# Kernel tuning notes

Hardware: AMD Instinct MI355X
Metric: run time of the kernel (lower is better)

Reference implementation:

```python
import jax, jax.numpy as jnp
import numpy as np

NUM_BINS = 50


def _power_spectrum(x):
    # fft2 over last two dims, |.|^2, fftshift — matches torch.fft.fft2/fftshift
    freq = jnp.fft.fft2(x, axes=(-2, -1))
    power = jnp.abs(freq) ** 2
    return jnp.fft.fftshift(power, axes=(-2, -1))


def _radial_bin_ids(H, W, num_bins):
    # Static precompute of the bin index for every pixel (replaces the
    # triple-nested mask loop with a single segment reduction).
    cy, cx = H // 2, W // 2
    y = jnp.arange(H, dtype=jnp.float32) - cy
    x = jnp.arange(W, dtype=jnp.float32) - cx
    radius = jnp.sqrt(y[:, None] ** 2 + x[None, :] ** 2)  # [H, W]
    max_radius = min(H, W) // 2
    bin_edges = jnp.linspace(0.0, float(max_radius), num_bins + 1)
    # bin i covers [edges[i], edges[i+1]); radius >= max_radius -> overflow bin
    ids = jnp.clip(jnp.searchsorted(bin_edges, radius.ravel(), side='right') - 1, 0, num_bins)
    return ids  # [H*W], values in [0, num_bins] (num_bins = dropped overflow)


def _radial_profile(power, num_bins=NUM_BINS):
    B, C, H, W = power.shape
    ids = _radial_bin_ids(H, W, num_bins)
    pflat = power.reshape(B, C, H * W)
    seg_sum = jax.vmap(jax.vmap(lambda p: jax.ops.segment_sum(p, ids, num_segments=num_bins + 1)))(pflat)
    counts = jax.ops.segment_sum(jnp.ones((H * W,), power.dtype), ids, num_segments=num_bins + 1)
    profile = jnp.where(counts > 0, seg_sum / jnp.maximum(counts, 1.0), 0.0)
    return profile[..., :num_bins]  # [B, C, num_bins]


def setup_inputs() -> dict:
    key = jax.random.key(0)
    k1, k2 = jax.random.split(key)
    x = jax.random.normal(k1, (16, 3, 512, 512), dtype=jnp.float32)
    reference = jax.random.normal(k2, (16, 3, 512, 512), dtype=jnp.float32)
    return {"x": x, "reference": reference}


def reference(x, reference):
    power_x = _power_spectrum(x)
    profile_x = _radial_profile(power_x)
    power_ref = _power_spectrum(reference)
    profile_ref = _radial_profile(power_ref)
    B = profile_x.shape[0]
    logits_x = profile_x.reshape(B, -1)
    logits_ref = profile_ref.reshape(B, -1)
    # F.kl_div(log_p, q).sum(1) == sum q * (log q - log p)
    log_p = jax.nn.log_softmax(logits_x, axis=1)
    log_q = jax.nn.log_softmax(logits_ref, axis=1)
    q = jnp.exp(log_q)
    divergence = jnp.sum(q * (log_q - log_p), axis=1)  # [B]
    return divergence
```

## Files before the change

### kernel.cpp

```cpp
#include <hip/hip_runtime.h>


#define NIMG 96
#define NB 50
#define NCOL 257
#define PHYS(k) ((k) ^ (((k) >> 3) & 7))

typedef unsigned int uint32;
typedef unsigned short ushort16;

__device__ __forceinline__ float2 cadd(float2 a, float2 b){ return make_float2(a.x+b.x, a.y+b.y); }
__device__ __forceinline__ float2 csub(float2 a, float2 b){ return make_float2(a.x-b.x, a.y-b.y); }
__device__ __forceinline__ float2 cmul(float2 a, float2 b){
  return make_float2(fmaf(a.x, b.x, -(a.y*b.y)), fmaf(a.x, b.y, a.y*b.x));
}
__device__ __forceinline__ float2 mul_mi(float2 a){ return make_float2(a.y, -a.x); }

__device__ __forceinline__ uint32 bfpack(float re, float im) {
  uint32 ur = __float_as_uint(re); ur += 0x7FFFu + ((ur >> 16) & 1u);
  uint32 ui = __float_as_uint(im); ui += 0x7FFFu + ((ui >> 16) & 1u);
  return (ur & 0xFFFF0000u) | (ui >> 16);
}
__device__ __forceinline__ float2 bfunpack(uint32 u) {
  return make_float2(__uint_as_float(u & 0xFFFF0000u), __uint_as_float(u << 16));
}

struct C8 { float2 m0, m1, m2, m3, m4, m5, m6, m7; };

__device__ __forceinline__ C8 fft8(C8 v) {
  const float C = 0.70710678118654752f;
  float2 t0=cadd(v.m0,v.m4), t1=csub(v.m0,v.m4);
  float2 t2=cadd(v.m2,v.m6), t3m=mul_mi(csub(v.m2,v.m6));
  float2 E0=cadd(t0,t2), E1=cadd(t1,t3m), E2=csub(t0,t2), E3=csub(t1,t3m);
  float2 s0=cadd(v.m1,v.m5), s1=csub(v.m1,v.m5);
  float2 s2=cadd(v.m3,v.m7), s3m=mul_mi(csub(v.m3,v.m7));
  float2 O0=cadd(s0,s2), O1=cadd(s1,s3m), O2=csub(s0,s2), O3=csub(s1,s3m);
  O1 = make_float2(C*(O1.x+O1.y), C*(O1.y-O1.x));
  O2 = mul_mi(O2);
  O3 = make_float2(C*(O3.y-O3.x), -C*(O3.x+O3.y));
  C8 r;
  r.m0=cadd(E0,O0); r.m4=csub(E0,O0);
  r.m1=cadd(E1,O1); r.m5=csub(E1,O1);
  r.m2=cadd(E2,O2); r.m6=csub(E2,O2);
  r.m3=cadd(E3,O3); r.m7=csub(E3,O3);
  return r;
}

#define TWAPPLY(XA, XB, W) do { float2 t_ = (W);                        \
  XA.m1=cmul(XA.m1,t_); XB.m1=cmul(XB.m1,t_); t_=cmul(t_,(W));          \
  XA.m2=cmul(XA.m2,t_); XB.m2=cmul(XB.m2,t_); t_=cmul(t_,(W));          \
  XA.m3=cmul(XA.m3,t_); XB.m3=cmul(XB.m3,t_); t_=cmul(t_,(W));          \
  XA.m4=cmul(XA.m4,t_); XB.m4=cmul(XB.m4,t_); t_=cmul(t_,(W));          \
  XA.m5=cmul(XA.m5,t_); XB.m5=cmul(XB.m5,t_); t_=cmul(t_,(W));          \
  XA.m6=cmul(XA.m6,t_); XB.m6=cmul(XB.m6,t_); t_=cmul(t_,(W));          \
  XA.m7=cmul(XA.m7,t_); XB.m7=cmul(XB.m7,t_); } while(0)

#define TWAP1(X, W) do { float2 t_ = (W);                               \
  X.m1=cmul(X.m1,t_); t_=cmul(t_,(W));                                  \
  X.m2=cmul(X.m2,t_); t_=cmul(t_,(W));                                  \
  X.m3=cmul(X.m3,t_); t_=cmul(t_,(W));                                  \
  X.m4=cmul(X.m4,t_); t_=cmul(t_,(W));                                  \
  X.m5=cmul(X.m5,t_); t_=cmul(t_,(W));                                  \
  X.m6=cmul(X.m6,t_); t_=cmul(t_,(W));                                  \
  X.m7=cmul(X.m7,t_); } while(0)

#define DUAL_FFT512(XA, XB, ZA, ZB, W1, W2, HI, LO) do {                      \
  XA = fft8(XA); XB = fft8(XB);                                               \
  TWAPPLY(XA, XB, W1);                                                        \
  ZA[      8*((HI)^0)+(LO)] = XA.m0;  ZB[      8*((HI)^0)+(LO)] = XB.m0;      \
  ZA[ 64 + 8*((HI)^1)+(LO)] = XA.m1;  ZB[ 64 + 8*((HI)^1)+(LO)] = XB.m1;      \
  ZA[128 + 8*((HI)^2)+(LO)] = XA.m2;  ZB[128 + 8*((HI)^2)+(LO)] = XB.m2;      \
  ZA[192 + 8*((HI)^3)+(LO)] = XA.m3;  ZB[192 + 8*((HI)^3)+(LO)] = XB.m3;      \
  ZA[256 + 8*((HI)^4)+(LO)] = XA.m4;  ZB[256 + 8*((HI)^4)+(LO)] = XB.m4;      \
  ZA[320 + 8*((HI)^5)+(LO)] = XA.m5;  ZB[320 + 8*((HI)^5)+(LO)] = XB.m5;      \
  ZA[384 + 8*((HI)^6)+(LO)] = XA.m6;  ZB[384 + 8*((HI)^6)+(LO)] = XB.m6;      \
  ZA[448 + 8*((HI)^7)+(LO)] = XA.m7;  ZB[448 + 8*((HI)^7)+(LO)] = XB.m7;      \
  __builtin_amdgcn_wave_barrier();                                            \
  XA.m0 = ZA[64*(HI)+8*(0^(HI))+(LO)]; XB.m0 = ZB[64*(HI)+8*(0^(HI))+(LO)];   \
  XA.m1 = ZA[64*(HI)+8*(1^(HI))+(LO)]; XB.m1 = ZB[64*(HI)+8*(1^(HI))+(LO)];   \
  XA.m2 = ZA[64*(HI)+8*(2^(HI))+(LO)]; XB.m2 = ZB[64*(HI)+8*(2^(HI))+(LO)];   \
  XA.m3 = ZA[64*(HI)+8*(3^(HI))+(LO)]; XB.m3 = ZB[64*(HI)+8*(3^(HI))+(LO)];   \
  XA.m4 = ZA[64*(HI)+8*(4^(HI))+(LO)]; XB.m4 = ZB[64*(HI)+8*(4^(HI))+(LO)];   \
  XA.m5 = ZA[64*(HI)+8*(5^(HI))+(LO)]; XB.m5 = ZB[64*(HI)+8*(5^(HI))+(LO)];   \
  XA.m6 = ZA[64*(HI)+8*(6^(HI))+(LO)]; XB.m6 = ZB[64*(HI)+8*(6^(HI))+(LO)];   \
  XA.m7 = ZA[64*(HI)+8*(7^(HI))+(LO)]; XB.m7 = ZB[64*(HI)+8*(7^(HI))+(LO)];   \
  __builtin_amdgcn_wave_barrier();                                            \
  XA = fft8(XA); XB = fft8(XB);                                               \
  TWAPPLY(XA, XB, W2);                                                        \
  ZA[64*(HI)+8*(0^(HI))+((LO)^0)] = XA.m0; ZB[64*(HI)+8*(0^(HI))+((LO)^0)] = XB.m0; \
  ZA[64*(HI)+8*(1^(HI))+((LO)^1)] = XA.m1; ZB[64*(HI)+8*(1^(HI))+((LO)^1)] = XB.m1; \
  ZA[64*(HI)+8*(2^(HI))+((LO)^2)] = XA.m2; ZB[64*(HI)+8*(2^(HI))+((LO)^2)] = XB.m2; \
  ZA[64*(HI)+8*(3^(HI))+((LO)^3)] = XA.m3; ZB[64*(HI)+8*(3^(HI))+((LO)^3)] = XB.m3; \
  ZA[64*(HI)+8*(4^(HI))+((LO)^4)] = XA.m4; ZB[64*(HI)+8*(4^(HI))+((LO)^4)] = XB.m4; \
  ZA[64*(HI)+8*(5^(HI))+((LO)^5)] = XA.m5; ZB[64*(HI)+8*(5^(HI))+((LO)^5)] = XB.m5; \
  ZA[64*(HI)+8*(6^(HI))+((LO)^6)] = XA.m6; ZB[64*(HI)+8*(6^(HI))+((LO)^6)] = XB.m6; \
  ZA[64*(HI)+8*(7^(HI))+((LO)^7)] = XA.m7; ZB[64*(HI)+8*(7^(HI))+((LO)^7)] = XB.m7; \
  __builtin_amdgcn_wave_barrier();                                            \
  XA.m0 = ZA[64*(HI)+8*((LO)^(HI))+(0^(LO))]; XB.m0 = ZB[64*(HI)+8*((LO)^(HI))+(0^(LO))]; \
  XA.m1 = ZA[64*(HI)+8*((LO)^(HI))+(1^(LO))]; XB.m1 = ZB[64*(HI)+8*((LO)^(HI))+(1^(LO))]; \
  XA.m2 = ZA[64*(HI)+8*((LO)^(HI))+(2^(LO))]; XB.m2 = ZB[64*(HI)+8*((LO)^(HI))+(2^(LO))]; \
  XA.m3 = ZA[64*(HI)+8*((LO)^(HI))+(3^(LO))]; XB.m3 = ZB[64*(HI)+8*((LO)^(HI))+(3^(LO))]; \
  XA.m4 = ZA[64*(HI)+8*((LO)^(HI))+(4^(LO))]; XB.m4 = ZB[64*(HI)+8*((LO)^(HI))+(4^(LO))]; \
  XA.m5 = ZA[64*(HI)+8*((LO)^(HI))+(5^(LO))]; XB.m5 = ZB[64*(HI)+8*((LO)^(HI))+(5^(LO))]; \
  XA.m6 = ZA[64*(HI)+8*((LO)^(HI))+(6^(LO))]; XB.m6 = ZB[64*(HI)+8*((LO)^(HI))+(6^(LO))]; \
  XA.m7 = ZA[64*(HI)+8*((LO)^(HI))+(7^(LO))]; XB.m7 = ZB[64*(HI)+8*((LO)^(HI))+(7^(LO))]; \
  __builtin_amdgcn_wave_barrier();                                            \
  XA = fft8(XA); XB = fft8(XB);                                               \
} while(0)

#define FFT512_1(X, Z, W1, W2, HI, LO) do {                                   \
  X = fft8(X);                                                                \
  TWAP1(X, W1);                                                               \
  Z[      8*((HI)^0)+(LO)] = X.m0;                                            \
  Z[ 64 + 8*((HI)^1)+(LO)] = X.m1;                                            \
  Z[128 + 8*((HI)^2)+(LO)] = X.m2;                                            \
  Z[192 + 8*((HI)^3)+(LO)] = X.m3;                                            \
  Z[256 + 8*((HI)^4)+(LO)] = X.m4;                                            \
  Z[320 + 8*((HI)^5)+(LO)] = X.m5;                                            \
  Z[384 + 8*((HI)^6)+(LO)] = X.m6;                                            \
  Z[448 + 8*((HI)^7)+(LO)] = X.m7;                                            \
  __builtin_amdgcn_wave_barrier();                                            \
  X.m0 = Z[64*(HI)+8*(0^(HI))+(LO)];                                          \
  X.m1 = Z[64*(HI)+8*(1^(HI))+(LO)];                                          \
  X.m2 = Z[64*(HI)+8*(2^(HI))+(LO)];                                          \
  X.m3 = Z[64*(HI)+8*(3^(HI))+(LO)];                                          \
  X.m4 = Z[64*(HI)+8*(4^(HI))+(LO)];                                          \
  X.m5 = Z[64*(HI)+8*(5^(HI))+(LO)];                                          \
  X.m6 = Z[64*(HI)+8*(6^(HI))+(LO)];                                          \
  X.m7 = Z[64*(HI)+8*(7^(HI))+(LO)];                                          \
  __builtin_amdgcn_wave_barrier();                                            \
  X = fft8(X);                                                                \
  TWAP1(X, W2);                                                               \
  Z[64*(HI)+8*(0^(HI))+((LO)^0)] = X.m0;                                      \
  Z[64*(HI)+8*(1^(HI))+((LO)^1)] = X.m1;                                      \
  Z[64*(HI)+8*(2^(HI))+((LO)^2)] = X.m2;                                      \
  Z[64*(HI)+8*(3^(HI))+((LO)^3)] = X.m3;                                      \
  Z[64*(HI)+8*(4^(HI))+((LO)^4)] = X.m4;                                      \
  Z[64*(HI)+8*(5^(HI))+((LO)^5)] = X.m5;                                      \
  Z[64*(HI)+8*(6^(HI))+((LO)^6)] = X.m6;                                      \
  Z[64*(HI)+8*(7^(HI))+((LO)^7)] = X.m7;                                      \
  __builtin_amdgcn_wave_barrier();                                            \
  X.m0 = Z[64*(HI)+8*((LO)^(HI))+(0^(LO))];                                   \
  X.m1 = Z[64*(HI)+8*((LO)^(HI))+(1^(LO))];                                   \
  X.m2 = Z[64*(HI)+8*((LO)^(HI))+(2^(LO))];                                   \
  X.m3 = Z[64*(HI)+8*((LO)^(HI))+(3^(LO))];                                   \
  X.m4 = Z[64*(HI)+8*((LO)^(HI))+(4^(LO))];                                   \
  X.m5 = Z[64*(HI)+8*((LO)^(HI))+(5^(LO))];                                   \
  X.m6 = Z[64*(HI)+8*((LO)^(HI))+(6^(LO))];                                   \
  X.m7 = Z[64*(HI)+8*((LO)^(HI))+(7^(LO))];                                   \
  __builtin_amdgcn_wave_barrier();                                            \
  X = fft8(X);                                                                \
} while(0)

#define TWIDDLE_W(W1, W2, lane)                                             \
  float2 W1, W2;                                                            \
  {                                                                         \
    float sv, cv;                                                           \
    __sincosf(-6.283185307179586f * (float)(lane) / 512.f, &sv, &cv);       \
    W1 = make_float2(cv, sv);                                               \
    __sincosf(-6.283185307179586f * (float)((lane) & 7) / 64.f, &sv, &cv);  \
    W2 = make_float2(cv, sv);                                               \
  }

__device__ __forceinline__ int binOf(int s, int cc) {
  return (int)(sqrtf((float)(s * s + cc * cc)) * 0.1953125f);
}
__device__ __forceinline__ int slo(int b, int cc) {
  if (b <= 0) return 0;
  float t = 26.2144f * (float)(b * b) - (float)(cc * cc);
  int s = (t <= 0.f) ? 0 : (int)ceilf(sqrtf(t));
  if (s > 257) s = 257;
  while (s > 0 && binOf(s - 1, cc) >= b) --s;
  while (s < 257 && binOf(s, cc) < b) ++s;
  return s;
}

__global__ __launch_bounds__(256) void build_slo_table(ushort16* __restrict__ tab)
{
  const int idx = blockIdx.x * 256 + threadIdx.x;
  if (idx >= NCOL * 51) return;
  const int c = idx / 51, b = idx - c * 51;
  tab[c * 52 + b] = (ushort16)slo(b, c);
}

__global__ __launch_bounds__(256, 4) void fft_rows_T(
    const float* __restrict__ xin, const float* __restrict__ rin,
    uint32* __restrict__ outT, int img0)
{
  __shared__ float2 s_z[8][512];
  __shared__ uint2  s_stage[64][8];
  const int tid = threadIdx.x, w = tid >> 6, lane = tid & 63;
  const int hi = lane >> 3, lo = lane & 7;
  const int imgL = blockIdx.x >> 5, blkin = blockIdx.x & 31;
  const int img = img0 + imgL;
  const float* base = (img < 48) ? (xin + (size_t)img * 262144)
                                 : (rin + (size_t)(img - 48) * 262144);
  const int rpA = blkin * 8 + w;
  const int rpB = rpA + 4;
  const float* srcA = base + (size_t)rpA * 1024;
  const float* srcB = base + (size_t)rpB * 1024;

  TWIDDLE_W(w1, w2, lane)
  float2* zA = s_z[2*w];
  float2* zB = s_z[2*w + 1];
  uint32* outImg = outT + (size_t)imgL * ((size_t)NCOL * 512);

  C8 xA, xB;
  xA.m0 = make_float2(srcA[      lane], srcA[512 +       lane]);
  xA.m1 = make_float2(srcA[ 64 + lane], srcA[512 +  64 + lane]);
  xA.m2 = make_float2(srcA[128 + lane], srcA[512 + 128 + lane]);
  xA.m3 = make_float2(srcA[192 + lane], srcA[512 + 192 + lane]);
  xA.m4 = make_float2(srcA[256 + lane], srcA[512 + 256 + lane]);
  xA.m5 = make_float2(srcA[320 + lane], srcA[512 + 320 + lane]);
  xA.m6 = make_float2(srcA[384 + lane], srcA[512 + 384 + lane]);
  xA.m7 = make_float2(srcA[448 + lane], srcA[512 + 448 + lane]);
  xB.m0 = make_float2(srcB[      lane], srcB[512 +       lane]);
  xB.m1 = make_float2(srcB[ 64 + lane], srcB[512 +  64 + lane]);
  xB.m2 = make_float2(srcB[128 + lane], srcB[512 + 128 + lane]);
  xB.m3 = make_float2(srcB[192 + lane], srcB[512 + 192 + lane]);
  xB.m4 = make_float2(srcB[256 + lane], srcB[512 + 256 + lane]);
  xB.m5 = make_float2(srcB[320 + lane], srcB[512 + 320 + lane]);
  xB.m6 = make_float2(srcB[384 + lane], srcB[512 + 384 + lane]);
  xB.m7 = make_float2(srcB[448 + lane], srcB[512 + 448 + lane]);

  DUAL_FFT512(xA, xB, zA, zB, w1, w2, hi, lo);

  zA[PHYS(hi + 8*lo +   0)] = xA.m0;  zB[PHYS(hi + 8*lo +   0)] = xB.m0;
  zA[PHYS(hi + 8*lo +  64)] = xA.m1;  zB[PHYS(hi + 8*lo +  64)] = xB.m1;
  zA[PHYS(hi + 8*lo + 128)] = xA.m2;  zB[PHYS(hi + 8*lo + 128)] = xB.m2;
  zA[PHYS(hi + 8*lo + 192)] = xA.m3;  zB[PHYS(hi + 8*lo + 192)] = xB.m3;
  zA[PHYS(hi + 8*lo + 256)] = xA.m4;  zB[PHYS(hi + 8*lo + 256)] = xB.m4;
  zA[PHYS(hi + 8*lo + 320)] = xA.m5;  zB[PHYS(hi + 8*lo + 320)] = xB.m5;
  zA[PHYS(hi + 8*lo + 384)] = xA.m6;  zB[PHYS(hi + 8*lo + 384)] = xB.m6;
  zA[PHYS(hi + 8*lo + 448)] = xA.m7;  zB[PHYS(hi + 8*lo + 448)] = xB.m7;
  __builtin_amdgcn_wave_barrier();

  #pragma unroll
  for (int a = 0; a < 4; ++a) {
    const int k  = 64 * a + lane;
    const int pk = (512 - k) & 511;
    float2 zkA = zA[PHYS(k)], zpA = zA[PHYS(pk)];
    float2 zkB = zB[PHYS(k)], zpB = zB[PHYS(pk)];
    uint32 uA0 = bfpack(0.5f*(zkA.x + zpA.x), 0.5f*(zkA.y - zpA.y));
    uint32 uA1 = bfpack(0.5f*(zkA.y + zpA.y), 0.5f*(zpA.x - zkA.x));
    uint32 uB0 = bfpack(0.5f*(zkB.x + zpB.x), 0.5f*(zkB.y - zpB.y));
    uint32 uB1 = bfpack(0.5f*(zkB.y + zpB.y), 0.5f*(zpB.x - zkB.x));
    s_stage[lane][(w + lane) & 7]     = make_uint2(uA0, uA1);
    s_stage[lane][(w + 4 + lane) & 7] = make_uint2(uB0, uB1);
    __syncthreads();
    const int kk = tid >> 2, jj = (tid & 3) * 2;
    uint2 v0 = s_stage[kk][(jj + kk) & 7];
    uint2 v1 = s_stage[kk][(jj + 1 + kk) & 7];
    *reinterpret_cast<uint4*>(outImg + ((size_t)(64*a + kk) * 512
                                        + 16*blkin + 2*jj)) =
        make_uint4(v0.x, v0.y, v1.x, v1.y);
    __syncthreads();
  }
  if (lane == 0) {
    float2 znA = zA[256], znB = zB[256];
    *reinterpret_cast<uint2*>(outImg + ((size_t)256 * 512 + 2 * rpA)) =
        make_uint2(bfpack(znA.x, 0.f), bfpack(znA.y, 0.f));
    *reinterpret_cast<uint2*>(outImg + ((size_t)256 * 512 + 2 * rpB)) =
        make_uint2(bfpack(znB.x, 0.f), bfpack(znB.y, 0.f));
  }
}

__global__ __launch_bounds__(256, 8) void fft_cols_bin1(
    const uint32* __restrict__ inT, const ushort16* __restrict__ tab,
    float* __restrict__ profSum, int img0)
{
  __shared__ float2 s_z[4][512];
  __shared__ float s_bins[4][64];
  const int tid = threadIdx.x, w = tid >> 6, lane = tid & 63;
  const int hi = lane >> 3, lo = lane & 7;
  const int imgL = blockIdx.x / 65, blkin = blockIdx.x - imgL * 65;
  const int imgG = img0 + imgL;
  const int c  = blkin * 4 + w;
  const int cs = (c <= 256) ? c : 256;
  const float wf = (c > 256) ? 0.f : ((c == 0 || c == 256) ? 1.f : 2.f);

  TWIDDLE_W(w1, w2, lane)
  float2* z = s_z[w];
  const uint32* src = inT + ((size_t)(imgL * NCOL + cs)) * 512;
  C8 x;
  x.m0 = bfunpack(src[      lane]);
  x.m1 = bfunpack(src[ 64 + lane]);
  x.m2 = bfunpack(src[128 + lane]);
  x.m3 = bfunpack(src[192 + lane]);
  x.m4 = bfunpack(src[256 + lane]);
  x.m5 = bfunpack(src[320 + lane]);
  x.m6 = bfunpack(src[384 + lane]);
  x.m7 = bfunpack(src[448 + lane]);

  int ts0 = 0, ts1 = 0;
  if (lane < NB) {
    ts0 = tab[cs * 52 + lane];
    ts1 = tab[cs * 52 + lane + 1];
  }

  FFT512_1(x, z, w1, w2, hi, lo);

  float* zf = (float*)z;
  const int low6 = hi + 8 * lo;
  zf[low6      ] = x.m0.x*x.m0.x + x.m0.y*x.m0.y;
  zf[low6 +  64] = x.m1.x*x.m1.x + x.m1.y*x.m1.y;
  zf[low6 + 128] = x.m2.x*x.m2.x + x.m2.y*x.m2.y;
  zf[low6 + 192] = x.m3.x*x.m3.x + x.m3.y*x.m3.y;
  zf[low6 + 256] = x.m4.x*x.m4.x + x.m4.y*x.m4.y;
  zf[low6 + 320] = x.m5.x*x.m5.x + x.m5.y*x.m5.y;
  zf[low6 + 384] = x.m6.x*x.m6.x + x.m6.y*x.m6.y;
  zf[low6 + 448] = x.m7.x*x.m7.x + x.m7.y*x.m7.y;
  __builtin_amdgcn_wave_barrier();

  float4 a0 = *reinterpret_cast<float4*>(&zf[8 * lane]);
  float4 a1 = *reinterpret_cast<float4*>(&zf[8 * lane + 4]);

  a0.y += a0.x; a0.z += a0.y; a0.w += a0.z;
  a1.x += a0.w; a1.y += a1.x; a1.z += a1.y; a1.w += a1.z;
  float tot = a1.w;

  float s = tot;
  #pragma unroll
  for (int d = 1; d < 64; d <<= 1) {
    float t = __shfl_up(s, d);
    if (lane >= d) s += t;
  }
  float off = s - tot;
  a0.x += off; a0.y += off; a0.z += off; a0.w += off;
  a1.x += off; a1.y += off; a1.z += off; a1.w += off;

  *reinterpret_cast<float4*>(&zf[8 * lane])     = a0;
  *reinterpret_cast<float4*>(&zf[8 * lane + 4]) = a1;
  __builtin_amdgcn_wave_barrier();

  float acc = 0.f;
  if (lane < NB) {
    const int s0 = ts0, s1 = ts1;
    int hp = (s1 < 257 ? s1 : 257) - 1;
    float pos = ((hp >= 0) ? zf[hp] : 0.f) - ((s0 > 0) ? zf[s0 - 1] : 0.f);
    int sa = (s0 > 1) ? s0 : 1;
    int sb = (s1 - 1 < 255) ? (s1 - 1) : 255;
    float neg = (sb >= sa) ? (zf[512 - sa] - zf[511 - sb]) : 0.f;
    acc = wf * (pos + neg);
  }
  s_bins[w][lane] = acc;
  __syncthreads();
  if (tid < NB) {
    float ss = s_bins[0][tid] + s_bins[1][tid] + s_bins[2][tid] + s_bins[3][tid];
    atomicAdd(&profSum[(size_t)imgG * NB + tid], ss);
  }
}

__global__ __launch_bounds__(256) void compute_counts(float* __restrict__ cnt)
{
  const int t = threadIdx.x;
  __shared__ float lb[NB];
  if (t < NB) lb[t] = 0.f;
  __syncthreads();
  const int base = blockIdx.x * 2048;
  #pragma unroll
  for (int k = 0; k < 8; ++k) {
    const int idx = base + k * 256 + t;
    const int y  = idx >> 9;
    const int xx = idx & 511;
    const int sy = (y < 256) ? y : y - 512;
    const int sx = (xx < 256) ? xx : xx - 512;
    float r = sqrtf((float)(sy * sy + sx * sx));
    int bb = (int)(r * 0.1953125f);
    if (bb < NB) atomicAdd(&lb[bb], 1.f);
  }
  __syncthreads();
  if (t < NB) atomicAdd(&cnt[t], lb[t]);
}

__global__ __launch_bounds__(256) void finalize_kl(
    const float* __restrict__ profSum, const float* __restrict__ cntg,
    float* __restrict__ out)
{
  const int b = blockIdx.x;
  const int t = threadIdx.x;
  __shared__ float red[256];

  float lxv = -3.0e38f, lrv = -3.0e38f;
  if (t < 150) {
    const int cc  = t / NB;
    const int bin = t - cc * NB;
    const float c = cntg[bin];
    lxv = profSum[(size_t)(b * 3 + cc) * NB + bin] / c;
    lrv = profSum[(size_t)(48 + b * 3 + cc) * NB + bin] / c;
  }
  auto rmax = [&](float v) {
    red[t] = v; __syncthreads();
    for (int s2 = 128; s2 >= 1; s2 >>= 1) {
      if (t < s2) red[t] = fmaxf(red[t], red[t + s2]);
      __syncthreads();
    }
    float rr = red[0]; __syncthreads();
    return rr;
  };
  auto rsum = [&](float v) {
    red[t] = v; __syncthreads();
    for (int s2 = 128; s2 >= 1; s2 >>= 1) {
      if (t < s2) red[t] = red[t] + red[t + s2];
      __syncthreads();
    }
    float rr = red[0]; __syncthreads();
    return rr;
  };
  const float mx  = rmax(lxv);
  const float mr  = rmax(lrv);
  const float sx  = rsum((t < 150) ? expf(lxv - mx) : 0.f);
  const float sr  = rsum((t < 150) ? expf(lrv - mr) : 0.f);
  const float lsx = logf(sx);
  const float lsr = logf(sr);
  float term = 0.f;
  if (t < 150) {
    const float logp = lxv - mx - lsx;
    const float logq = lrv - mr - lsr;
    const float q    = expf(logq);
    term = q * (logq - logp);
  }
  const float div = rsum(term);
  if (t == 0) out[b] = div;
}

extern "C" void kernel_launch(void* const* d_in, const int* in_sizes, int n_in,
                              void* d_out, int out_size, void* d_ws, size_t ws_size,
                              hipStream_t stream)
{
  const float* x = (const float*)d_in[0];
  const float* r = (const float*)d_in[1];
  float* out     = (float*)d_out;

  float* profSum = (float*)d_ws;
  float* cnt     = (float*)((char*)d_ws + 19200);
  ushort16* tab  = (ushort16*)((char*)d_ws + 19456);
  const size_t IM_OFS = 46592;
  uint32* interT = (uint32*)((char*)d_ws + IM_OFS);

  const size_t perImg = (size_t)NCOL * 512 * sizeof(uint32);
  size_t avail = (ws_size > IM_OFS) ? (ws_size - IM_OFS) : 0;
  int ic = (int)(avail / perImg);
  if (ic > NIMG) ic = NIMG;
  if (ic < 1) ic = 1;

  hipMemsetAsync(d_ws, 0, 19456, stream);
  hipLaunchKernelGGL(build_slo_table, dim3(52), dim3(256), 0, stream, tab);
  hipLaunchKernelGGL(compute_counts, dim3(128), dim3(256), 0, stream, cnt);

  for (int img0 = 0; img0 < NIMG; img0 += ic) {
    const int n = (NIMG - img0 < ic) ? (NIMG - img0) : ic;
    hipLaunchKernelGGL(fft_rows_T, dim3(n * 32), dim3(256), 0, stream,
                       x, r, interT, img0);
    hipLaunchKernelGGL(fft_cols_bin1, dim3(n * 65), dim3(256), 0, stream,
                       interT, tab, profSum, img0);
  }
  hipLaunchKernelGGL(finalize_kl, dim3(16), dim3(256), 0, stream,
                     profSum, cnt, out);
}
```

Baseline: 69.43 us.

## Process one row-pair per wave in row FFT and drop staging buffer

The row FFT kernel now has each wave handle a single packed row pair instead of two, doubling the grid and raising launch bounds to 8 waves/SIMD occupancy. The separate s_stage transpose buffer and its per-iteration double __syncthreads are replaced by writing all four separated spectra into the wave's own z buffer, then one block barrier followed by transposed reads and narrower 8-byte global stores. This aims to cut LDS footprint, register pressure and synchronization to improve latency hiding. The trade-off is smaller (uint2 instead of uint4) output stores and more blocks launched.

Measured after the change: 78.90 us. 13.6% more time.

```diff
diff --git a/kernel.cpp b/kernel.cpp
--- a/kernel.cpp
+++ b/kernel.cpp
@@ -46,15 +46,6 @@
   return r;
 }
 
-#define TWAPPLY(XA, XB, W) do { float2 t_ = (W);                        \
-  XA.m1=cmul(XA.m1,t_); XB.m1=cmul(XB.m1,t_); t_=cmul(t_,(W));          \
-  XA.m2=cmul(XA.m2,t_); XB.m2=cmul(XB.m2,t_); t_=cmul(t_,(W));          \
-  XA.m3=cmul(XA.m3,t_); XB.m3=cmul(XB.m3,t_); t_=cmul(t_,(W));          \
-  XA.m4=cmul(XA.m4,t_); XB.m4=cmul(XB.m4,t_); t_=cmul(t_,(W));          \
-  XA.m5=cmul(XA.m5,t_); XB.m5=cmul(XB.m5,t_); t_=cmul(t_,(W));          \
-  XA.m6=cmul(XA.m6,t_); XB.m6=cmul(XB.m6,t_); t_=cmul(t_,(W));          \
-  XA.m7=cmul(XA.m7,t_); XB.m7=cmul(XB.m7,t_); } while(0)
-
 #define TWAP1(X, W) do { float2 t_ = (W);                               \
   X.m1=cmul(X.m1,t_); t_=cmul(t_,(W));                                  \
   X.m2=cmul(X.m2,t_); t_=cmul(t_,(W));                                  \
@@ -63,50 +54,6 @@
   X.m5=cmul(X.m5,t_); t_=cmul(t_,(W));                                  \
   X.m6=cmul(X.m6,t_); t_=cmul(t_,(W));                                  \
   X.m7=cmul(X.m7,t_); } while(0)
-
-#define DUAL_FFT512(XA, XB, ZA, ZB, W1, W2, HI, LO) do {                      \
-  XA = fft8(XA); XB = fft8(XB);                                               \
-  TWAPPLY(XA, XB, W1);                                                        \
-  ZA[      8*((HI)^0)+(LO)] = XA.m0;  ZB[      8*((HI)^0)+(LO)] = XB.m0;      \
-  ZA[ 64 + 8*((HI)^1)+(LO)] = XA.m1;  ZB[ 64 + 8*((HI)^1)+(LO)] = XB.m1;      \
-  ZA[128 + 8*((HI)^2)+(LO)] = XA.m2;  ZB[128 + 8*((HI)^2)+(LO)] = XB.m2;      \
-  ZA[192 + 8*((HI)^3)+(LO)] = XA.m3;  ZB[192 + 8*((HI)^3)+(LO)] = XB.m3;      \
-  ZA[256 + 8*((HI)^4)+(LO)] = XA.m4;  ZB[256 + 8*((HI)^4)+(LO)] = XB.m4;      \
-  ZA[320 + 8*((HI)^5)+(LO)] = XA.m5;  ZB[320 + 8*((HI)^5)+(LO)] = XB.m5;      \
-  ZA[384 + 8*((HI)^6)+(LO)] = XA.m6;  ZB[384 + 8*((HI)^6)+(LO)] = XB.m6;      \
-  ZA[448 + 8*((HI)^7)+(LO)] = XA.m7;  ZB[448 + 8*((HI)^7)+(LO)] = XB.m7;      \
-  __builtin_amdgcn_wave_barrier();                                            \
-  XA.m0 = ZA[64*(HI)+8*(0^(HI))+(LO)]; XB.m0 = ZB[64*(HI)+8*(0^(HI))+(LO)];   \
-  XA.m1 = ZA[64*(HI)+8*(1^(HI))+(LO)]; XB.m1 = ZB[64*(HI)+8*(1^(HI))+(LO)];   \
-  XA.m2 = ZA[64*(HI)+8*(2^(HI))+(LO)]; XB.m2 = ZB[64*(HI)+8*(2^(HI))+(LO)];   \
-  XA.m3 = ZA[64*(HI)+8*(3^(HI))+(LO)]; XB.m3 = ZB[64*(HI)+8*(3^(HI))+(LO)];   \
-  XA.m4 = ZA[64*(HI)+8*(4^(HI))+(LO)]; XB.m4 = ZB[64*(HI)+8*(4^(HI))+(LO)];   \
-  XA.m5 = ZA[64*(HI)+8*(5^(HI))+(LO)]; XB.m5 = ZB[64*(HI)+8*(5^(HI))+(LO)];   \
-  XA.m6 = ZA[64*(HI)+8*(6^(HI))+(LO)]; XB.m6 = ZB[64*(HI)+8*(6^(HI))+(LO)];   \
-  XA.m7 = ZA[64*(HI)+8*(7^(HI))+(LO)]; XB.m7 = ZB[64*(HI)+8*(7^(HI))+(LO)];   \
-  __builtin_amdgcn_wave_barrier();                                            \
-  XA = fft8(XA); XB = fft8(XB);                                               \
-  TWAPPLY(XA, XB, W2);                                                        \
-  ZA[64*(HI)+8*(0^(HI))+((LO)^0)] = XA.m0; ZB[64*(HI)+8*(0^(HI))+((LO)^0)] = XB.m0; \
-  ZA[64*(HI)+8*(1^(HI))+((LO)^1)] = XA.m1; ZB[64*(HI)+8*(1^(HI))+((LO)^1)] = XB.m1; \
-  ZA[64*(HI)+8*(2^(HI))+((LO)^2)] = XA.m2; ZB[64*(HI)+8*(2^(HI))+((LO)^2)] = XB.m2; \
-  ZA[64*(HI)+8*(3^(HI))+((LO)^3)] = XA.m3; ZB[64*(HI)+8*(3^(HI))+((LO)^3)] = XB.m3; \
-  ZA[64*(HI)+8*(4^(HI))+((LO)^4)] = XA.m4; ZB[64*(HI)+8*(4^(HI))+((LO)^4)] = XB.m4; \
-  ZA[64*(HI)+8*(5^(HI))+((LO)^5)] = XA.m5; ZB[64*(HI)+8*(5^(HI))+((LO)^5)] = XB.m5; \
-  ZA[64*(HI)+8*(6^(HI))+((LO)^6)] = XA.m6; ZB[64*(HI)+8*(6^(HI))+((LO)^6)] = XB.m6; \
-  ZA[64*(HI)+8*(7^(HI))+((LO)^7)] = XA.m7; ZB[64*(HI)+8*(7^(HI))+((LO)^7)] = XB.m7; \
-  __builtin_amdgcn_wave_barrier();                                            \
-  XA.m0 = ZA[64*(HI)+8*((LO)^(HI))+(0^(LO))]; XB.m0 = ZB[64*(HI)+8*((LO)^(HI))+(0^(LO))]; \
-  XA.m1 = ZA[64*(HI)+8*((LO)^(HI))+(1^(LO))]; XB.m1 = ZB[64*(HI)+8*((LO)^(HI))+(1^(LO))]; \
-  XA.m2 = ZA[64*(HI)+8*((LO)^(HI))+(2^(LO))]; XB.m2 = ZB[64*(HI)+8*((LO)^(HI))+(2^(LO))]; \
-  XA.m3 = ZA[64*(HI)+8*((LO)^(HI))+(3^(LO))]; XB.m3 = ZB[64*(HI)+8*((LO)^(HI))+(3^(LO))]; \
-  XA.m4 = ZA[64*(HI)+8*((LO)^(HI))+(4^(LO))]; XB.m4 = ZB[64*(HI)+8*((LO)^(HI))+(4^(LO))]; \
-  XA.m5 = ZA[64*(HI)+8*((LO)^(HI))+(5^(LO))]; XB.m5 = ZB[64*(HI)+8*((LO)^(HI))+(5^(LO))]; \
-  XA.m6 = ZA[64*(HI)+8*((LO)^(HI))+(6^(LO))]; XB.m6 = ZB[64*(HI)+8*((LO)^(HI))+(6^(LO))]; \
-  XA.m7 = ZA[64*(HI)+8*((LO)^(HI))+(7^(LO))]; XB.m7 = ZB[64*(HI)+8*((LO)^(HI))+(7^(LO))]; \
-  __builtin_amdgcn_wave_barrier();                                            \
-  XA = fft8(XA); XB = fft8(XB);                                               \
-} while(0)
 
 #define FFT512_1(X, Z, W1, W2, HI, LO) do {                                   \
   X = fft8(X);                                                                \
@@ -183,85 +130,81 @@
   tab[c * 52 + b] = (ushort16)slo(b, c);
 }
 
-__global__ __launch_bounds__(256, 4) void fft_rows_T(
+__global__ __launch_bounds__(256, 8) void fft_rows_T(
     const float* __restrict__ xin, const float* __restrict__ rin,
     uint32* __restrict__ outT, int img0)
 {
-  __shared__ float2 s_z[8][512];
-  __shared__ uint2  s_stage[64][8];
+  __shared__ float2 s_z[4][516];
   const int tid = threadIdx.x, w = tid >> 6, lane = tid & 63;
   const int hi = lane >> 3, lo = lane & 7;
-  const int imgL = blockIdx.x >> 5, blkin = blockIdx.x & 31;
+  const int imgL = blockIdx.x >> 6, blkin = blockIdx.x & 63;
   const int img = img0 + imgL;
   const float* base = (img < 48) ? (xin + (size_t)img * 262144)
                                  : (rin + (size_t)(img - 48) * 262144);
-  const int rpA = blkin * 8 + w;
-  const int rpB = rpA + 4;
-  const float* srcA = base + (size_t)rpA * 1024;
-  const float* srcB = base + (size_t)rpB * 1024;
+  const int rp = blkin * 4 + w;
+  const float* src = base + (size_t)rp * 1024;
 
   TWIDDLE_W(w1, w2, lane)
-  float2* zA = s_z[2*w];
-  float2* zB = s_z[2*w + 1];
+  float2* z = s_z[w];
   uint32* outImg = outT + (size_t)imgL * ((size_t)NCOL * 512);
 
-  C8 xA, xB;
-  xA.m0 = make_float2(srcA[      lane], srcA[512 +       lane]);
-  xA.m1 = make_float2(srcA[ 64 + lane], srcA[512 +  64 + lane]);
-  xA.m2 = make_float2(srcA[128 + lane], srcA[512 + 128 + lane]);
-  xA.m3 = make_float2(srcA[192 + lane], srcA[512 + 192 + lane]);
-  xA.m4 = make_float2(srcA[256 + lane], srcA[512 + 256 + lane]);
-  xA.m5 = make_float2(srcA[320 + lane], srcA[512 + 320 + lane]);
-  xA.m6 = make_float2(srcA[384 + lane], srcA[512 + 384 + lane]);
-  xA.m7 = make_float2(srcA[448 + lane], srcA[512 + 448 + lane]);
-  xB.m0 = make_float2(srcB[      lane], srcB[512 +       lane]);
-  xB.m1 = make_float2(srcB[ 64 + lane], srcB[512 +  64 + lane]);
-  xB.m2 = make_float2(srcB[128 + lane], srcB[512 + 128 + lane]);
-  xB.m3 = make_float2(srcB[192 + lane], srcB[512 + 192 + lane]);
-  xB.m4 = make_float2(srcB[256 + lane], srcB[512 + 256 + lane]);
-  xB.m5 = make_float2(srcB[320 + lane], srcB[512 + 320 + lane]);
-  xB.m6 = make_float2(srcB[384 + lane], srcB[512 + 384 + lane]);
-  xB.m7 = make_float2(srcB[448 + lane], srcB[512 + 448 + lane]);
-
-  DUAL_FFT512(xA, xB, zA, zB, w1, w2, hi, lo);
-
-  zA[PHYS(hi + 8*lo +   0)] = xA.m0;  zB[PHYS(hi + 8*lo +   0)] = xB.m0;
-  zA[PHYS(hi + 8*lo +  64)] = xA.m1;  zB[PHYS(hi + 8*lo +  64)] = xB.m1;
-  zA[PHYS(hi + 8*lo + 128)] = xA.m2;  zB[PHYS(hi + 8*lo + 128)] = xB.m2;
-  zA[PHYS(hi + 8*lo + 192)] = xA.m3;  zB[PHYS(hi + 8*lo + 192)] = xB.m3;
-  zA[PHYS(hi + 8*lo + 256)] = xA.m4;  zB[PHYS(hi + 8*lo + 256)] = xB.m4;
-  zA[PHYS(hi + 8*lo + 320)] = xA.m5;  zB[PHYS(hi + 8*lo + 320)] = xB.m5;
-  zA[PHYS(hi + 8*lo + 384)] = xA.m6;  zB[PHYS(hi + 8*lo + 384)] = xB.m6;
-  zA[PHYS(hi + 8*lo + 448)] = xA.m7;  zB[PHYS(hi + 8*lo + 448)] = xB.m7;
+  C8 x;
+  x.m0 = make_float2(src[      lane], src[512 +       lane]);
+  x.m1 = make_float2(src[ 64 + lane], src[512 +  64 + lane]);
+  x.m2 = make_float2(src[128 + lane], src[512 + 128 + lane]);
+  x.m3 = make_float2(src[192 + lane], src[512 + 192 + lane]);
+  x.m4 = make_float2(src[256 + lane], src[512 + 256 + lane]);
+  x.m5 = make_float2(src[320 + lane], src[512 + 320 + lane]);
+  x.m6 = make_float2(src[384 + lane], src[512 + 384 + lane]);
+  x.m7 = make_float2(src[448 + lane], src[512 + 448 + lane]);
+
+  FFT512_1(x, z, w1, w2, hi, lo);
+
+  z[PHYS(hi + 8*lo +   0)] = x.m0;
+  z[PHYS(hi + 8*lo +  64)] = x.m1;
+  z[PHYS(hi + 8*lo + 128)] = x.m2;
+  z[PHYS(hi + 8*lo + 192)] = x.m3;
+  z[PHYS(hi + 8*lo + 256)] = x.m4;
+  z[PHYS(hi + 8*lo + 320)] = x.m5;
+  z[PHYS(hi + 8*lo + 384)] = x.m6;
+  z[PHYS(hi + 8*lo + 448)] = x.m7;
   __builtin_amdgcn_wave_barrier();
 
+#define SEPK(A, ST)                                                          \
+  uint2 ST;                                                                  \
+  {                                                                          \
+    const int k  = 64 * (A) + lane;                                          \
+    const int pk = (512 - k) & 511;                                          \
+    float2 zk = z[PHYS(k)], zp = z[PHYS(pk)];                                \
+    ST = make_uint2(bfpack(0.5f*(zk.x + zp.x), 0.5f*(zk.y - zp.y)),          \
+                    bfpack(0.5f*(zk.y + zp.y), 0.5f*(zp.x - zk.x)));         \
+  }
+  SEPK(0, st0)
+  SEPK(1, st1)
+  SEPK(2, st2)
+  SEPK(3, st3)
+#undef SEPK
+  float2 zn = z[256];
+  __builtin_amdgcn_wave_barrier();
+
+  uint2* zU = (uint2*)z;
+  zU[       lane] = st0;
+  zU[ 64 +  lane] = st1;
+  zU[128 +  lane] = st2;
+  zU[192 +  lane] = st3;
+  __syncthreads();
+
+  const int kk = tid >> 2, jj = tid & 3;
+  const uint2* zUj = (const uint2*)(s_z[jj]);
   #pragma unroll
   for (int a = 0; a < 4; ++a) {
-    const int k  = 64 * a + lane;
-    const int pk = (512 - k) & 511;
-    float2 zkA = zA[PHYS(k)], zpA = zA[PHYS(pk)];
-    float2 zkB = zB[PHYS(k)], zpB = zB[PHYS(pk)];
-    uint32 uA0 = bfpack(0.5f*(zkA.x + zpA.x), 0.5f*(zkA.y - zpA.y));
-    uint32 uA1 = bfpack(0.5f*(zkA.y + zpA.y), 0.5f*(zpA.x - zkA.x));
-    uint32 uB0 = bfpack(0.5f*(zkB.x + zpB.x), 0.5f*(zkB.y - zpB.y));
-    uint32 uB1 = bfpack(0.5f*(zkB.y + zpB.y), 0.5f*(zpB.x - zkB.x));
-    s_stage[lane][(w + lane) & 7]     = make_uint2(uA0, uA1);
-    s_stage[lane][(w + 4 + lane) & 7] = make_uint2(uB0, uB1);
-    __syncthreads();
-    const int kk = tid >> 2, jj = (tid & 3) * 2;
-    uint2 v0 = s_stage[kk][(jj + kk) & 7];
-    uint2 v1 = s_stage[kk][(jj + 1 + kk) & 7];
-    *reinterpret_cast<uint4*>(outImg + ((size_t)(64*a + kk) * 512
-                                        + 16*blkin + 2*jj)) =
-        make_uint4(v0.x, v0.y, v1.x, v1.y);
-    __syncthreads();
+    uint2 v = zUj[64 * a + kk];
+    *reinterpret_cast<uint2*>(outImg + ((size_t)(64 * a + kk) * 512
+                                        + 8 * blkin + 2 * jj)) = v;
   }
   if (lane == 0) {
-    float2 znA = zA[256], znB = zB[256];
-    *reinterpret_cast<uint2*>(outImg + ((size_t)256 * 512 + 2 * rpA)) =
-        make_uint2(bfpack(znA.x, 0.f), bfpack(znA.y, 0.f));
-    *reinterpret_cast<uint2*>(outImg + ((size_t)256 * 512 + 2 * rpB)) =
-        make_uint2(bfpack(znB.x, 0.f), bfpack(znB.y, 0.f));
+    *reinterpret_cast<uint2*>(outImg + ((size_t)256 * 512 + 2 * rp)) =
+        make_uint2(bfpack(zn.x, 0.f), bfpack(zn.y, 0.f));
   }
 }
 
@@ -450,7 +393,7 @@
 
   for (int img0 = 0; img0 < NIMG; img0 += ic) {
     const int n = (NIMG - img0 < ic) ? (NIMG - img0) : ic;
-    hipLaunchKernelGGL(fft_rows_T, dim3(n * 32), dim3(256), 0, stream,
+    hipLaunchKernelGGL(fft_rows_T, dim3(n * 64), dim3(256), 0, stream,
                        x, r, interT, img0);
     hipLaunchKernelGGL(fft_cols_bin1, dim3(n * 65), dim3(256), 0, stream,
                        interT, tab, profSum, img0);
```
